# Optimization experiments

Measured on AMD Instinct MI355X. Metric: run time of the kernel, lower is better.

## Reference

```python
import jax, jax.numpy as jnp
import numpy as np

K_NEIGHBORS = 20


def _glorot(key, shape):
    fan_in = shape[0]
    return jax.random.normal(key, shape, dtype=jnp.float32) / jnp.sqrt(jnp.float32(fan_in))


def setup_inputs() -> dict:
    key = jax.random.key(0)
    ks = jax.random.split(key, 20)
    B, N, D = 16, 1024, 3
    out_channels = 40
    pos = jax.random.normal(ks[0], (B, N, D), dtype=jnp.float32)
    inp = {
        "pos": pos,
        # conv1 MLP: [6 -> 64 -> 64 -> 64]
        "W1a": _glorot(ks[1], (6, 64)),   "b1a": jnp.zeros((64,), jnp.float32),
        "W1b": _glorot(ks[2], (64, 64)),  "b1b": jnp.zeros((64,), jnp.float32),
        "W1c": _glorot(ks[3], (64, 64)),  "b1c": jnp.zeros((64,), jnp.float32),
        # conv2 MLP: [128 -> 128]
        "W2": _glorot(ks[4], (128, 128)), "b2": jnp.zeros((128,), jnp.float32),
        # lin1: 64+128 -> 1024
        "Wl": _glorot(ks[5], (192, 1024)), "bl": jnp.zeros((1024,), jnp.float32),
        # head MLP: [1024 -> 512 -> 256 -> out]
        "Wm1": _glorot(ks[6], (1024, 512)), "bm1": jnp.zeros((512,), jnp.float32),
        "Wm2": _glorot(ks[7], (512, 256)),  "bm2": jnp.zeros((256,), jnp.float32),
        "Wm3": _glorot(ks[8], (256, out_channels)), "bm3": jnp.zeros((out_channels,), jnp.float32),
    }
    return inp


def _knn_idx(x, k):
    # x: [B, N, D] -> idx: [B, N, k] of nearest neighbors (self excluded)
    sq = jnp.sum(x * x, axis=-1)                      # [B, N]
    d = sq[:, :, None] + sq[:, None, :] - 2.0 * jnp.einsum("bnd,bmd->bnm", x, x)
    n = x.shape[1]
    d = d + jnp.eye(n, dtype=d.dtype)[None] * jnp.float32(1e10)  # exclude self
    _, idx = jax.lax.top_k(-d, k)                     # smallest distances
    return idx


def _edge_conv(x, k, mlp_fn):
    # DynamicEdgeConv: kNN graph on current features, message = mlp([x_i, x_j - x_i]), max-aggr.
    idx = _knn_idx(x, k)                              # [B, N, k]
    nb = jax.vmap(lambda xb, ib: xb[ib])(x, idx)      # [B, N, k, C] gather
    xi = jnp.broadcast_to(x[:, :, None, :], nb.shape)
    e = jnp.concatenate([xi, nb - xi], axis=-1)       # [B, N, k, 2C]
    return jnp.max(mlp_fn(e), axis=2)                 # max over neighbors -> [B, N, C']


def reference(pos, W1a, b1a, W1b, b1b, W1c, b1c, W2, b2, Wl, bl,
              Wm1, bm1, Wm2, bm2, Wm3, bm3):
    relu = jax.nn.relu
    # conv1: MLP([6,64,64,64]) -- ReLU after hidden layers, plain last (eval: BN identity, dropout off)
    mlp1 = lambda e: relu(relu(e @ W1a + b1a) @ W1b + b1b) @ W1c + b1c
    x1 = _edge_conv(pos, K_NEIGHBORS, mlp1)           # [B, N, 64]
    # conv2: MLP([128,128]) -- single plain linear
    x2 = _edge_conv(x1, K_NEIGHBORS, lambda e: e @ W2 + b2)  # [B, N, 128]
    out = jnp.concatenate([x1, x2], axis=-1) @ Wl + bl       # [B, N, 1024]
    g = jnp.max(out, axis=1)                                  # global max pool -> [B, 1024]
    h = relu(g @ Wm1 + bm1)
    h = relu(h @ Wm2 + bm2)
    logits = h @ Wm3 + bm3                                    # [B, 40]
    return jax.nn.log_softmax(logits, axis=1)
```

## Files before the change

kernel.cpp:

```cpp
#include <hip/hip_runtime.h>

constexpr int NB  = 16;
constexpr int NP  = 1024;
constexpr int NPT = NB * NP;
constexpr int KNB = 20;

typedef unsigned short ushortT;
typedef __bf16 bf16x8 __attribute__((ext_vector_type(8)));
typedef _Float16 f16x8 __attribute__((ext_vector_type(8)));
typedef float f32x4 __attribute__((ext_vector_type(4)));

__device__ inline unsigned f2bf_pair(float f0, float f1) {
    unsigned u0 = __float_as_uint(f0); u0 = (u0 + 0x7FFFu + ((u0 >> 16) & 1u)) >> 16;
    unsigned u1 = __float_as_uint(f1); u1 = (u1 + 0x7FFFu + ((u1 >> 16) & 1u)) >> 16;
    return u0 | (u1 << 16);
}

__device__ inline unsigned monokey(float f) {
    unsigned u = __float_as_uint(f);
    return u ^ ((unsigned)((int)u >> 31) | 0x80000000u);
}

__device__ inline unsigned dppmin16(unsigned v) {
    unsigned t;
    t = (unsigned)__builtin_amdgcn_update_dpp((int)v, (int)v, 0xB1, 0xF, 0xF, false);
    v = v < t ? v : t;
    t = (unsigned)__builtin_amdgcn_update_dpp((int)v, (int)v, 0x4E, 0xF, 0xF, false);
    v = v < t ? v : t;
    t = (unsigned)__builtin_amdgcn_update_dpp((int)v, (int)v, 0x141, 0xF, 0xF, false);
    v = v < t ? v : t;
    t = (unsigned)__builtin_amdgcn_update_dpp((int)v, (int)v, 0x140, 0xF, 0xF, false);
    v = v < t ? v : t;
    return v;
}

__device__ inline void sort16_u64(unsigned long long key[16]) {
#pragma unroll
    for (int k = 2; k <= 16; k <<= 1) {
#pragma unroll
        for (int j = k >> 1; j > 0; j >>= 1) {
#pragma unroll
            for (int a = 0; a < 16; ++a) {
                int b = a ^ j;
                if (b > a) {
                    unsigned long long x = key[a], y = key[b];
                    bool lt = x < y;
                    unsigned long long mn = lt ? x : y, mx = lt ? y : x;
                    if ((a & k) == 0) { key[a] = mn; key[b] = mx; }
                    else              { key[a] = mx; key[b] = mn; }
                }
            }
        }
    }
}

__device__ inline void wave_top20_lds(unsigned long long key[16], int lane,
                                      unsigned long long* __restrict__ col,
                                      int* __restrict__ outp, int jadd)
{
    sort16_u64(key);
#pragma unroll
    for (int s = 0; s < 16; ++s) col[s] = key[s];
    unsigned ptr = 0;
    for (int t = 0; t < KNB; ++t) {
        unsigned long long h = col[ptr];
        unsigned hv = (unsigned)(h >> 32);
        unsigned hj = (unsigned)h;
        unsigned r = dppmin16(hv);
        unsigned g0 = (unsigned)__builtin_amdgcn_readlane((int)r, 0);
        unsigned g1 = (unsigned)__builtin_amdgcn_readlane((int)r, 16);
        unsigned g2 = (unsigned)__builtin_amdgcn_readlane((int)r, 32);
        unsigned g3 = (unsigned)__builtin_amdgcn_readlane((int)r, 48);
        unsigned g = min(min(g0, g1), min(g2, g3));
        unsigned long long ball = __ballot(hv == g);
        int wl = __ffsll(ball) - 1;
        int wj = __builtin_amdgcn_readlane((int)hj, wl);
        if (lane == 0) outp[t] = jadd + wj;
        ptr += (lane == wl) ? 1u : 0u;
    }
}

__device__ inline void tourney20(unsigned long long key[16], int lane,
                                 unsigned long long* __restrict__ heap,
                                 int* __restrict__ outp, int jadd)
{
    sort16_u64(key);
#pragma unroll
    for (int s = 0; s < 16; ++s)
        heap[lane * 16 + ((s + lane) & 15)] = key[s];
    unsigned ptr = 0;
    for (int t = 0; t < KNB; ++t) {
        unsigned pcl = ptr < 15u ? ptr : 15u;
        unsigned long long h = heap[lane * 16 + (((int)pcl + lane) & 15)];
        if (ptr >= 16u) h = ~0ULL;
        unsigned hv = (unsigned)(h >> 32);
        unsigned hj = (unsigned)h;
        unsigned r = dppmin16(hv);
        unsigned g0 = (unsigned)__builtin_amdgcn_readlane((int)r, 0);
        unsigned g1 = (unsigned)__builtin_amdgcn_readlane((int)r, 16);
        unsigned g2 = (unsigned)__builtin_amdgcn_readlane((int)r, 32);
        unsigned g3 = (unsigned)__builtin_amdgcn_readlane((int)r, 48);
        unsigned g = min(min(g0, g1), min(g2, g3));
        unsigned long long ball = __ballot(hv == g);
        int wl = __ffsll(ball) - 1;
        int wj = __builtin_amdgcn_readlane((int)hj, wl);
        if (lane == 0) outp[t] = jadd + wj;
        ptr += (lane == wl) ? 1u : 0u;
    }
}

__global__ void fail_kernel(float* out, int n) {
    int i = blockIdx.x * 256 + threadIdx.x;
    if (i < n) out[i] = -777.0f;
}

__global__ __launch_bounds__(256) void prep_w_kernel(
    const float* __restrict__ W2,
    const float* __restrict__ Wm1, const float* __restrict__ Wm2, const float* __restrict__ Wm3,
    const float* __restrict__ Wl, const float* __restrict__ W1b, const float* __restrict__ W1c,
    float* __restrict__ Wcat, float* __restrict__ Wm1T, float* __restrict__ Wm2T, float* __restrict__ Wm3T,
    ushortT* __restrict__ Wlb, _Float16* __restrict__ Wc1f)
{
    int id = blockIdx.x * 256 + threadIdx.x;
    if (id < 64 * 256) {
        int c = id >> 8, n = id & 255;
        float wb = W2[(64 + c) * 128 + (n & 127)];
        Wcat[id] = (n < 128) ? wb : (W2[c * 128 + (n - 128)] - wb);
        return;
    }
    id -= 64 * 256;
    if (id < 512 * 1024) { int j = id >> 10, c = id & 1023; Wm1T[id] = Wm1[c * 512 + j]; return; }
    id -= 512 * 1024;
    if (id < 256 * 512)  { int j = id >> 9,  c = id & 511;  Wm2T[id] = Wm2[c * 256 + j]; return; }
    id -= 256 * 512;
    if (id < 40 * 256)   { int j = id >> 8,  c = id & 255;  Wm3T[id] = Wm3[c * 40 + j];  return; }
    id -= 40 * 256;
    if (id < 8 * 6 * 8 * 64 * 8) {
        int j = id & 7;
        int t = id >> 3;
        int lane = t & 63; t >>= 6;
        int f = t & 7; t >>= 3;
        int s = t % 6, nt = t / 6;
        int k = s * 32 + (lane >> 4) * 8 + j;
        int n = nt * 128 + f * 16 + (lane & 15);
        unsigned u = __float_as_uint(Wl[(size_t)k * 1024 + n]);
        u = (u + 0x7FFFu + ((u >> 16) & 1u)) >> 16;
        Wlb[id] = (ushortT)u;
        return;
    }
    id -= 8 * 6 * 8 * 64 * 8;
    if (id < 16384) {
        int mat = id >> 13;
        int rem = id & 8191;
        int part = rem >> 12;
        int t = rem & 4095;
        int frag = t >> 9;
        int r = t & 511;
        int lane = r >> 3, j = r & 7;
        int kf = frag >> 2, nf = frag & 3;
        int k = kf * 32 + (lane >> 4) * 8 + j;
        int n = nf * 16 + (lane & 15);
        float w = (mat ? W1c : W1b)[k * 64 + n];
        _Float16 hi = (_Float16)w;
        Wc1f[id] = part ? (_Float16)(w - (float)hi) : hi;
        return;
    }
}

__global__ __launch_bounds__(256) void prep_uv1_kernel(
    const float* __restrict__ pos, const float* __restrict__ W1a, const float* __restrict__ b1a,
    float* __restrict__ u1, float* __restrict__ v1)
{
    int id = blockIdx.x * 256 + threadIdx.x;
    int i = id >> 6, c = id & 63;
    float x = pos[3 * i], y = pos[3 * i + 1], z = pos[3 * i + 2];
    float wu0 = W1a[3 * 64 + c], wu1 = W1a[4 * 64 + c], wu2 = W1a[5 * 64 + c];
    float wv0 = W1a[0 * 64 + c] - wu0, wv1 = W1a[1 * 64 + c] - wu1, wv2 = W1a[2 * 64 + c] - wu2;
    u1[id] = x * wu0 + y * wu1 + z * wu2;
    v1[id] = b1a[c] + x * wv0 + y * wv1 + z * wv2;
}

__global__ __launch_bounds__(256) void knn3_kernel(const float* __restrict__ pos, int* __restrict__ idx)
{
    __shared__ unsigned long long heap[4][64][17];
    const int tid = threadIdx.x;
    const int w = tid >> 6, lane = tid & 63;
    const int b = blockIdx.x >> 8;
    const int i = ((blockIdx.x & 255) << 2) + w;
    const float* pb = pos + (size_t)b * NP * 3;

    float cbuf[48];
    {
        const float4* src = (const float4*)(pb + lane * 48);
#pragma unroll
        for (int q = 0; q < 12; ++q) *(float4*)&cbuf[q * 4] = src[q];
    }
    const float xi = pb[3 * i], yi = pb[3 * i + 1], zi = pb[3 * i + 2];
    const float sqi = xi * xi + yi * yi + zi * zi;
    unsigned long long key[16];
#pragma unroll
    for (int s = 0; s < 16; ++s) {
        float x = cbuf[3 * s], y = cbuf[3 * s + 1], z = cbuf[3 * s + 2];
        float d = sqi + (x * x + y * y + z * z) - 2.0f * (xi * x + yi * y + zi * z);
        int j = (lane << 4) + s;
        if (j == i) d += 1e10f;
        key[s] = ((unsigned long long)monokey(d) << 32) | (unsigned)j;
    }
    heap[w][lane][16] = ~0ULL;
    wave_top20_lds(key, lane, &heap[w][lane][0], idx + (size_t)(b * NP + i) * KNB, b * NP);
}

__global__ __launch_bounds__(64, 1) void conv1_mfma_kernel(
    const int* __restrict__ idx, const float* __restrict__ u1, const float* __restrict__ v1,
    const _Float16* __restrict__ Wf, const float* __restrict__ b1b, const float* __restrict__ b1c,
    float* __restrict__ x1)
{
    __shared__ int idx_s[16 * 20];
    __shared__ __align__(16) float tr[16 * 68];
    __shared__ __align__(16) float xout[16 * 68];
    const int lane = threadIdx.x;
    const int row = lane & 15, ks = lane >> 4;
    const int pbase = blockIdx.x * 16;

    for (int t = lane; t < 320; t += 64) idx_s[t] = idx[(size_t)pbase * 20 + t];

    const f16x8* Wp = (const f16x8*)Wf;
    f16x8 wbh[2][4], wbl[2][4], wch[2][4], wcl[2][4];
#pragma unroll
    for (int kf = 0; kf < 2; ++kf)
#pragma unroll
        for (int nf = 0; nf < 4; ++nf) {
            int f = kf * 4 + nf;
            wbh[kf][nf] = Wp[(0 * 8 + f) * 64 + lane];
            wbl[kf][nf] = Wp[(1 * 8 + f) * 64 + lane];
            wch[kf][nf] = Wp[(2 * 8 + f) * 64 + lane];
            wcl[kf][nf] = Wp[(3 * 8 + f) * 64 + lane];
        }
    float bb[4], bc[4];
#pragma unroll
    for (int nf = 0; nf < 4; ++nf) { bb[nf] = b1b[nf * 16 + row]; bc[nf] = b1c[nf * 16 + row]; }

    const int P = pbase + row;
    float4 v1f[4];
    {
        const float4* v4a = (const float4*)(v1 + (size_t)P * 64 + ks * 8);
        v1f[0] = v4a[0]; v1f[1] = v4a[1];
        const float4* v4b = (const float4*)(v1 + (size_t)P * 64 + 32 + ks * 8);
        v1f[2] = v4b[0]; v1f[3] = v4b[1];
    }
    f32x4 xmax[4];
#pragma unroll
    for (int nf = 0; nf < 4; ++nf) xmax[nf] = (f32x4)(-3.0e38f);

    int jn = idx_s[row * 20];
    float4 un[4];
    {
        const float4* up = (const float4*)(u1 + (size_t)jn * 64 + ks * 8);
        un[0] = up[0]; un[1] = up[1];
        const float4* up2 = (const float4*)(u1 + (size_t)jn * 64 + 32 + ks * 8);
        un[2] = up2[0]; un[3] = up2[1];
    }
    for (int e = 0; e < 20; ++e) {
        float4 uc[4] = {un[0], un[1], un[2], un[3]};
        if (e < 19) {
            jn = idx_s[row * 20 + e + 1];
            const float4* up = (const float4*)(u1 + (size_t)jn * 64 + ks * 8);
            un[0] = up[0]; un[1] = up[1];
            const float4* up2 = (const float4*)(u1 + (size_t)jn * 64 + 32 + ks * 8);
            un[2] = up2[0]; un[3] = up2[1];
        }
        f32x4 c2[4];
#pragma unroll
        for (int nf = 0; nf < 4; ++nf) c2[nf] = (f32x4)(bb[nf]);
#pragma unroll
        for (int kf = 0; kf < 2; ++kf) {
            const float* uu = (const float*)&uc[kf * 2];
            const float* vv = (const float*)&v1f[kf * 2];
            f16x8 ah, al;
#pragma unroll
            for (int q = 0; q < 8; ++q) {
                float h = fmaxf(uu[q] + vv[q], 0.f);
                _Float16 hi = (_Float16)h;
                ah[q] = hi;
                al[q] = (_Float16)(h - (float)hi);
            }
#pragma unroll
            for (int nf = 0; nf < 4; ++nf) {
                c2[nf] = __builtin_amdgcn_mfma_f32_16x16x32_f16(ah, wbh[kf][nf], c2[nf], 0, 0, 0);
                c2[nf] = __builtin_amdgcn_mfma_f32_16x16x32_f16(ah, wbl[kf][nf], c2[nf], 0, 0, 0);
                c2[nf] = __builtin_amdgcn_mfma_f32_16x16x32_f16(al, wbh[kf][nf], c2[nf], 0, 0, 0);
            }
        }
#pragma unroll
        for (int nf = 0; nf < 4; ++nf)
#pragma unroll
            for (int r = 0; r < 4; ++r)
                tr[(ks * 4 + r) * 68 + nf * 16 + row] = fmaxf(c2[nf][r], 0.f);
        __builtin_amdgcn_sched_barrier(0);
        f32x4 c3[4];
#pragma unroll
        for (int nf = 0; nf < 4; ++nf) c3[nf] = (f32x4)0.0f;
#pragma unroll
        for (int kf = 0; kf < 2; ++kf) {
            float hbuf[8];
            *(float4*)&hbuf[0] = *(const float4*)&tr[row * 68 + kf * 32 + ks * 8];
            *(float4*)&hbuf[4] = *(const float4*)&tr[row * 68 + kf * 32 + ks * 8 + 4];
            f16x8 ah, al;
#pragma unroll
            for (int q = 0; q < 8; ++q) {
                _Float16 hi = (_Float16)hbuf[q];
                ah[q] = hi;
                al[q] = (_Float16)(hbuf[q] - (float)hi);
            }
#pragma unroll
            for (int nf = 0; nf < 4; ++nf) {
                c3[nf] = __builtin_amdgcn_mfma_f32_16x16x32_f16(ah, wch[kf][nf], c3[nf], 0, 0, 0);
                c3[nf] = __builtin_amdgcn_mfma_f32_16x16x32_f16(ah, wcl[kf][nf], c3[nf], 0, 0, 0);
                c3[nf] = __builtin_amdgcn_mfma_f32_16x16x32_f16(al, wch[kf][nf], c3[nf], 0, 0, 0);
            }
        }
        __builtin_amdgcn_sched_barrier(0);
#pragma unroll
        for (int nf = 0; nf < 4; ++nf) {
            xmax[nf][0] = fmaxf(xmax[nf][0], c3[nf][0]);
            xmax[nf][1] = fmaxf(xmax[nf][1], c3[nf][1]);
            xmax[nf][2] = fmaxf(xmax[nf][2], c3[nf][2]);
            xmax[nf][3] = fmaxf(xmax[nf][3], c3[nf][3]);
        }
    }
#pragma unroll
    for (int nf = 0; nf < 4; ++nf)
#pragma unroll
        for (int r = 0; r < 4; ++r)
            xout[(ks * 4 + r) * 68 + nf * 16 + row] = xmax[nf][r] + bc[nf];
    __builtin_amdgcn_sched_barrier(0);
    {
        const int r2 = lane >> 2, c0 = (lane & 3) * 16;
#pragma unroll
        for (int q = 0; q < 4; ++q) {
            float4 v = *(const float4*)&xout[r2 * 68 + c0 + q * 4];
            *(float4*)(x1 + (size_t)(pbase + r2) * 64 + c0 + q * 4) = v;
        }
    }
}

__global__ __launch_bounds__(256) void sqnorm_kernel(
    const float* __restrict__ x1, float* __restrict__ sq,
    ushortT* __restrict__ Afrag, _Float16* __restrict__ Xf)
{
    int i = blockIdx.x * 256 + threadIdx.x;
    const float4* r = (const float4*)(x1 + (size_t)i * 64);
    float c[64];
    float s = 0.f;
#pragma unroll
    for (int q = 0; q < 16; ++q) {
        float4 a = r[q];
        c[4 * q] = a.x; c[4 * q + 1] = a.y; c[4 * q + 2] = a.z; c[4 * q + 3] = a.w;
        s += a.x * a.x + a.y * a.y + a.z * a.z + a.w * a.w;
    }
    sq[i] = s;
    const size_t t = i >> 4;
#pragma unroll
    for (int cb = 0; cb < 8; ++cb) {
        uint4 pk;
        pk.x = f2bf_pair(c[8 * cb + 0], c[8 * cb + 1]);
        pk.y = f2bf_pair(c[8 * cb + 2], c[8 * cb + 3]);
        pk.z = f2bf_pair(c[8 * cb + 4], c[8 * cb + 5]);
        pk.w = f2bf_pair(c[8 * cb + 6], c[8 * cb + 7]);
        size_t af = (t * 6 + (cb >> 2)) * 512 + (size_t)((cb & 3) * 16 + (i & 15)) * 8;
        *(uint4*)(Afrag + af) = pk;
        int kf = cb >> 2;
        int lanef = ((cb & 3) << 4) + (i & 15);
        __align__(16) _Float16 hbuf[8];
        __align__(16) _Float16 lbuf[8];
#pragma unroll
        for (int q2 = 0; q2 < 8; ++q2) {
            float v = c[cb * 8 + q2];
            _Float16 hi = (_Float16)v;
            hbuf[q2] = hi;
            lbuf[q2] = (_Float16)(v - (float)hi);
        }
        *(uint4*)(Xf + ((t * 2 + kf) * 2 + 0) * 512 + (size_t)lanef * 8) = *(uint4*)hbuf;
        *(uint4*)(Xf + ((t * 2 + kf) * 2 + 1) * 512 + (size_t)lanef * 8) = *(uint4*)lbuf;
    }
}

__global__ __launch_bounds__(512, 4) void dist2sel_kernel(
    const _Float16* __restrict__ Xf, const float* __restrict__ sq, int* __restrict__ idx)
{
    __shared__ unsigned kls[16 * 1032];
    const int tid = threadIdx.x;
    const int w = tid >> 6, lane = tid & 63;
    const int b = blockIdx.x >> 6;
    const int rowtile = blockIdx.x & 63;
    const int c15 = lane & 15;
    const int rbase = (lane >> 4) * 4;

    const f16x8* Xv = (const f16x8*)Xf;
    const int tA = b * 64 + rowtile;
    f16x8 ah[2], al[2];
#pragma unroll
    for (int kf = 0; kf < 2; ++kf) {
        ah[kf] = Xv[((size_t)(tA * 2 + kf) * 2 + 0) * 64 + lane];
        al[kf] = Xv[((size_t)(tA * 2 + kf) * 2 + 1) * 64 + lane];
    }
    const float* sqb = sq + (size_t)b * NP;
    float sqi[4];
#pragma unroll
    for (int rr = 0; rr < 4; ++rr)
        sqi[rr] = sqb[rowtile * 16 + rbase + rr];

    for (int q = 0; q < 8; ++q) {
        const int ct = w * 8 + q;
        const int tB = b * 64 + ct;
        f16x8 bh0 = Xv[((size_t)(tB * 2 + 0) * 2 + 0) * 64 + lane];
        f16x8 bl0 = Xv[((size_t)(tB * 2 + 0) * 2 + 1) * 64 + lane];
        f16x8 bh1 = Xv[((size_t)(tB * 2 + 1) * 2 + 0) * 64 + lane];
        f16x8 bl1 = Xv[((size_t)(tB * 2 + 1) * 2 + 1) * 64 + lane];
        const int col = ct * 16 + c15;
        const float sqj = sqb[col];
        f32x4 acc = (f32x4)0.0f;
        acc = __builtin_amdgcn_mfma_f32_16x16x32_f16(ah[0], bh0, acc, 0, 0, 0);
        acc = __builtin_amdgcn_mfma_f32_16x16x32_f16(ah[0], bl0, acc, 0, 0, 0);
        acc = __builtin_amdgcn_mfma_f32_16x16x32_f16(al[0], bh0, acc, 0, 0, 0);
        acc = __builtin_amdgcn_mfma_f32_16x16x32_f16(ah[1], bh1, acc, 0, 0, 0);
        acc = __builtin_amdgcn_mfma_f32_16x16x32_f16(ah[1], bl1, acc, 0, 0, 0);
        acc = __builtin_amdgcn_mfma_f32_16x16x32_f16(al[1], bh1, acc, 0, 0, 0);
        const int pc = col ^ (((col >> 6) & 7) << 1);
#pragma unroll
        for (int rr = 0; rr < 4; ++rr) {
            float d = sqi[rr] + sqj - 2.0f * acc[rr];
            if (rowtile * 16 + rbase + rr == col) d += 1e10f;
            kls[(rbase + rr) * 1032 + pc] = monokey(d);
        }
    }
    __syncthreads();

    const int r0 = 2 * w, r1 = 2 * w + 1;
    unsigned kv0[16], kv1[16];
#pragma unroll
    for (int s = 0; s < 16; ++s) {
        int col = (lane << 4) + s;
        int pc = col ^ (((col >> 6) & 7) << 1);
        kv0[s] = kls[r0 * 1032 + pc];
        kv1[s] = kls[r1 * 1032 + pc];
    }
    unsigned long long* heap = (unsigned long long*)&kls[(size_t)w * 2 * 1032];
    const int gb = b * NP;
    {
        unsigned long long key[16];
#pragma unroll
        for (int s = 0; s < 16; ++s)
            key[s] = ((unsigned long long)kv0[s] << 32) | (unsigned)((lane << 4) + s);
        tourney20(key, lane, heap, idx + (size_t)(gb + rowtile * 16 + r0) * KNB, gb);
    }
    {
        unsigned long long key[16];
#pragma unroll
        for (int s = 0; s < 16; ++s)
            key[s] = ((unsigned long long)kv1[s] << 32) | (unsigned)((lane << 4) + s);
        tourney20(key, lane, heap, idx + (size_t)(gb + rowtile * 16 + r1) * KNB, gb);
    }
}

__global__ __launch_bounds__(256) void u2v2_kernel(
    const float* __restrict__ x1, const float* __restrict__ Wcat, const float* __restrict__ b2,
    float* __restrict__ u2, float* __restrict__ v2)
{
    __shared__ float aT[32][132];
    __shared__ float bW[32][132];
    const int tid = threadIdx.x;
    const int mt = blockIdx.x >> 1, nt = blockIdx.x & 1;
    const int m0 = mt << 7, n0 = nt << 7;
    const int ti = tid >> 4, tj = tid & 15;
    float acc[8][8];
#pragma unroll
    for (int a = 0; a < 8; ++a)
#pragma unroll
        for (int q = 0; q < 8; ++q) acc[a][q] = 0.f;
    for (int ct = 0; ct < 2; ++ct) {
        __syncthreads();
#pragma unroll
        for (int rep = 0; rep < 4; ++rep) {
            int f = tid + (rep << 8);
            { int r = f >> 3, q = f & 7;
              float4 v = *(const float4*)(x1 + (size_t)(m0 + r) * 64 + ct * 32 + q * 4);
              aT[4 * q + 0][r] = v.x; aT[4 * q + 1][r] = v.y; aT[4 * q + 2][r] = v.z; aT[4 * q + 3][r] = v.w; }
            { int cc = f >> 5, q = f & 31;
              *(float4*)&bW[cc][4 * q] = *(const float4*)(Wcat + (size_t)(ct * 32 + cc) * 256 + n0 + q * 4); }
        }
        __syncthreads();
#pragma unroll 4
        for (int c = 0; c < 32; ++c) {
            float af[8], bf[8];
            *(float4*)&af[0] = *(const float4*)&aT[c][ti * 8];
            *(float4*)&af[4] = *(const float4*)&aT[c][ti * 8 + 4];
            *(float4*)&bf[0] = *(const float4*)&bW[c][tj * 8];
            *(float4*)&bf[4] = *(const float4*)&bW[c][tj * 8 + 4];
#pragma unroll
            for (int a = 0; a < 8; ++a)
#pragma unroll
                for (int q = 0; q < 8; ++q) acc[a][q] = fmaf(af[a], bf[q], acc[a][q]);
        }
    }
#pragma unroll
    for (int a = 0; a < 8; ++a) {
        int m = m0 + ti * 8 + a;
        if (n0 < 128) {
            float outv[8];
#pragma unroll
            for (int q = 0; q < 8; ++q) outv[q] = acc[a][q];
            *(float4*)(u2 + (size_t)m * 128 + n0 + tj * 8)     = *(float4*)&outv[0];
            *(float4*)(u2 + (size_t)m * 128 + n0 + tj * 8 + 4) = *(float4*)&outv[4];
        } else {
            float outv[8];
#pragma unroll
            for (int q = 0; q < 8; ++q) outv[q] = acc[a][q] + b2[n0 - 128 + tj * 8 + q];
            *(float4*)(v2 + (size_t)m * 128 + (n0 - 128) + tj * 8)     = *(float4*)&outv[0];
            *(float4*)(v2 + (size_t)m * 128 + (n0 - 128) + tj * 8 + 4) = *(float4*)&outv[4];
        }
    }
}

__global__ __launch_bounds__(256) void gatherfrag_kernel(
    const int* __restrict__ idx, const float* __restrict__ u2,
    const float* __restrict__ v2, ushortT* __restrict__ Afrag)
{
    const int tid = threadIdx.x;
    const int i = blockIdx.x * 16 + (tid >> 4);
    const int cb = tid & 15;
    const int* ib = idx + (size_t)i * KNB;
    float m[8];
#pragma unroll
    for (int d = 0; d < 8; ++d) m[d] = -3e38f;
    for (int e = 0; e < KNB; ++e) {
        int j = ib[e];
        const float4* p = (const float4*)(u2 + (size_t)j * 128 + cb * 8);
        float4 a = p[0], b = p[1];
        m[0] = fmaxf(m[0], a.x); m[1] = fmaxf(m[1], a.y); m[2] = fmaxf(m[2], a.z); m[3] = fmaxf(m[3], a.w);
        m[4] = fmaxf(m[4], b.x); m[5] = fmaxf(m[5], b.y); m[6] = fmaxf(m[6], b.z); m[7] = fmaxf(m[7], b.w);
    }
    const float4* vp = (const float4*)(v2 + (size_t)i * 128 + cb * 8);
    float4 va = vp[0], vb = vp[1];
    m[0] += va.x; m[1] += va.y; m[2] += va.z; m[3] += va.w;
    m[4] += vb.x; m[5] += vb.y; m[6] += vb.z; m[7] += vb.w;
    uint4 pk;
    pk.x = f2bf_pair(m[0], m[1]);
    pk.y = f2bf_pair(m[2], m[3]);
    pk.z = f2bf_pair(m[4], m[5]);
    pk.w = f2bf_pair(m[6], m[7]);
    size_t af = ((size_t)(i >> 4) * 6 + 2 + (cb >> 2)) * 512 + (size_t)((cb & 3) * 16 + (i & 15)) * 8;
    *(uint4*)(Afrag + af) = pk;
}

__global__ __launch_bounds__(256) void lin1max_mfma_kernel(
    const ushortT* __restrict__ Afrag, const ushortT* __restrict__ Wlb, float* __restrict__ gp)
{
    __shared__ float red[4][128];
    const int tid = threadIdx.x;
    const int w = tid >> 6, lane = tid & 63;
    const int nt = blockIdx.x & 7;
    const int rt = (blockIdx.x >> 3) & 7;
    const int b  = blockIdx.x >> 6;
    const int rt16 = ((b << 3) + rt) * 8 + (w << 1);
    const bf16x8* Ap = (const bf16x8*)Afrag;
    const bf16x8* Bp = (const bf16x8*)Wlb;
    f32x4 acc[2][8];
#pragma unroll
    for (int mm = 0; mm < 2; ++mm)
#pragma unroll
        for (int f = 0; f < 8; ++f) acc[mm][f] = (f32x4)0.0f;
#pragma unroll
    for (int s = 0; s < 6; ++s) {
        bf16x8 a0 = Ap[((rt16    ) * 6 + s) * 64 + lane];
        bf16x8 a1 = Ap[((rt16 + 1) * 6 + s) * 64 + lane];
#pragma unroll
        for (int f = 0; f < 8; ++f) {
            bf16x8 bb = Bp[(((nt * 6 + s) << 3) + f) * 64 + lane];
            acc[0][f] = __builtin_amdgcn_mfma_f32_16x16x32_bf16(a0, bb, acc[0][f], 0, 0, 0);
            acc[1][f] = __builtin_amdgcn_mfma_f32_16x16x32_bf16(a1, bb, acc[1][f], 0, 0, 0);
        }
    }
#pragma unroll
    for (int f = 0; f < 8; ++f) {
        float m = acc[0][f][0];
        m = fmaxf(m, acc[0][f][1]); m = fmaxf(m, acc[0][f][2]); m = fmaxf(m, acc[0][f][3]);
        m = fmaxf(m, acc[1][f][0]); m = fmaxf(m, acc[1][f][1]);
        m = fmaxf(m, acc[1][f][2]); m = fmaxf(m, acc[1][f][3]);
        m = fmaxf(m, __shfl_xor(m, 16, 64));
        m = fmaxf(m, __shfl_xor(m, 32, 64));
        if (lane < 16) red[w][f * 16 + lane] = m;
    }
    __syncthreads();
    if (tid < 128) {
        float m = fmaxf(fmaxf(red[0][tid], red[1][tid]), fmaxf(red[2][tid], red[3][tid]));
        gp[((size_t)rt * NB + b) * 1024 + nt * 128 + tid] = m;
    }
}

__global__ __launch_bounds__(256) void gmax_kernel(
    const float* __restrict__ gp, const float* __restrict__ bl, float* __restrict__ gs)
{
    int id = blockIdx.x * 256 + threadIdx.x;
    int b = id >> 10, c = id & 1023;
    float m = gp[(size_t)b * 1024 + c];
#pragma unroll
    for (int part = 1; part < 8; ++part)
        m = fmaxf(m, gp[((size_t)part * NB + b) * 1024 + c]);
    gs[(size_t)b * 1024 + c] = m + bl[c];
}

__global__ __launch_bounds__(256) void head1_kernel(
    const float* __restrict__ gs, const float* __restrict__ Wm1T, const float* __restrict__ bm1,
    float* __restrict__ h1)
{
    __shared__ float red[16][17];
    const int j = blockIdx.x;
    const int t = threadIdx.x;
    const int b = t >> 4, seg = t & 15;
    const float4* wr = (const float4*)(Wm1T + (size_t)j * 1024 + seg * 64);
    const float4* gr = (const float4*)(gs + (size_t)b * 1024 + seg * 64);
    float acc = 0.f;
#pragma unroll
    for (int q = 0; q < 16; ++q) {
        float4 w = wr[q], g = gr[q];
        acc = fmaf(w.x, g.x, acc); acc = fmaf(w.y, g.y, acc);
        acc = fmaf(w.z, g.z, acc); acc = fmaf(w.w, g.w, acc);
    }
    red[b][seg] = acc;
    __syncthreads();
    if (t < 16) {
        float s = 0.f;
#pragma unroll
        for (int k = 0; k < 16; ++k) s += red[t][k];
        h1[(size_t)t * 512 + j] = fmaxf(s + bm1[j], 0.f);
    }
}

__global__ __launch_bounds__(256) void head2_kernel(
    const float* __restrict__ h1, const float* __restrict__ Wm2T, const float* __restrict__ bm2,
    float* __restrict__ h2)
{
    __shared__ float red[16][17];
    const int j = blockIdx.x;
    const int t = threadIdx.x;
    const int b = t >> 4, seg = t & 15;
    const float4* wr = (const float4*)(Wm2T + (size_t)j * 512 + seg * 32);
    const float4* hr = (const float4*)(h1 + (size_t)b * 512 + seg * 32);
    float acc = 0.f;
#pragma unroll
    for (int q = 0; q < 8; ++q) {
        float4 w = wr[q], g = hr[q];
        acc = fmaf(w.x, g.x, acc); acc = fmaf(w.y, g.y, acc);
        acc = fmaf(w.z, g.z, acc); acc = fmaf(w.w, g.w, acc);
    }
    red[b][seg] = acc;
    __syncthreads();
    if (t < 16) {
        float s = 0.f;
#pragma unroll
        for (int k = 0; k < 16; ++k) s += red[t][k];
        h2[(size_t)t * 256 + j] = fmaxf(s + bm2[j], 0.f);
    }
}

__global__ __launch_bounds__(256) void head3_kernel(
    const float* __restrict__ h2, const float* __restrict__ Wm3T, const float* __restrict__ bm3,
    float* __restrict__ out)
{
    __shared__ float lg[64];
    const int tid = threadIdx.x;
    const int b = blockIdx.x;
    if (tid < 40) {
        float acc = bm3[tid];
        const float4* wr = (const float4*)(Wm3T + (size_t)tid * 256);
        const float4* hr = (const float4*)(h2 + (size_t)b * 256);
#pragma unroll
        for (int c4 = 0; c4 < 64; ++c4) {
            float4 w = wr[c4];
            float4 g4 = hr[c4];
            acc = fmaf(w.x, g4.x, acc); acc = fmaf(w.y, g4.y, acc);
            acc = fmaf(w.z, g4.z, acc); acc = fmaf(w.w, g4.w, acc);
        }
        lg[tid] = acc;
    }
    __syncthreads();
    if (tid < 64) {
        float v = (tid < 40) ? lg[tid] : -3e38f;
        float m = v;
        for (int off = 32; off; off >>= 1) m = fmaxf(m, __shfl_xor(m, off, 64));
        float ex = (tid < 40) ? expf(v - m) : 0.f;
        float s = ex;
        for (int off = 32; off; off >>= 1) s += __shfl_xor(s, off, 64);
        if (tid < 40) out[b * 40 + tid] = v - m - logf(s);
    }
}

extern "C" void kernel_launch(void* const* d_in, const int* in_sizes, int n_in,
                              void* d_out, int out_size, void* d_ws, size_t ws_size,
                              hipStream_t stream)
{
    const float* pos = (const float*)d_in[0];
    const float* W1a = (const float*)d_in[1];
    const float* b1a = (const float*)d_in[2];
    const float* W1b = (const float*)d_in[3];
    const float* b1b = (const float*)d_in[4];
    const float* W1c = (const float*)d_in[5];
    const float* b1c = (const float*)d_in[6];
    const float* W2  = (const float*)d_in[7];
    const float* b2  = (const float*)d_in[8];
    const float* Wl  = (const float*)d_in[9];
    const float* bl  = (const float*)d_in[10];
    const float* Wm1 = (const float*)d_in[11];
    const float* bm1 = (const float*)d_in[12];
    const float* Wm2 = (const float*)d_in[13];
    const float* bm2 = (const float*)d_in[14];
    const float* Wm3 = (const float*)d_in[15];
    const float* bm3 = (const float*)d_in[16];
    float* out = (float*)d_out;

    char* ws = (char*)d_ws;
    const size_t MB = 1024 * 1024;
    size_t off = 0;
    auto alloc = [&](size_t bytes) { size_t o = off; off += (bytes + 255) & ~(size_t)255; return o; };
    size_t u2_off  = alloc(8 * MB);
    size_t v2_off  = alloc(8 * MB);
    size_t x1_off  = alloc(4 * MB);
    size_t idx_off = alloc((size_t)NPT * KNB * 4);
    size_t sq_off  = alloc((size_t)NPT * 4);
    size_t gp_off  = alloc((size_t)8 * NB * 1024 * 4);
    size_t gs_off  = alloc((size_t)NB * 1024 * 4);
    size_t h1_off  = alloc((size_t)NB * 512 * 4);
    size_t h2_off  = alloc((size_t)NB * 256 * 4);
    size_t wc_off  = alloc(64 * 256 * 4);
    size_t w1t_off = alloc(512 * 1024 * 4);
    size_t w2t_off = alloc(256 * 512 * 4);
    size_t w3t_off = alloc(40 * 256 * 4);
    size_t af_off  = alloc((size_t)(NPT / 16) * 6 * 512 * 2);
    size_t wlb_off = alloc((size_t)8 * 6 * 8 * 512 * 2);
    size_t wcf_off = alloc((size_t)16384 * 2);
    size_t xf_off  = alloc((size_t)(NPT / 16) * 2 * 2 * 512 * 2);
    if (ws_size < off) { fail_kernel<<<3, 256, 0, stream>>>(out, out_size); return; }

    float* u1    = (float*)(ws + u2_off);
    float* v1    = (float*)(ws + v2_off);
    float* u2    = (float*)(ws + u2_off);
    float* v2    = (float*)(ws + v2_off);
    float* x1    = (float*)(ws + x1_off);
    int*   idx   = (int*)(ws + idx_off);
    float* sq    = (float*)(ws + sq_off);
    float* gp    = (float*)(ws + gp_off);
    float* gs    = (float*)(ws + gs_off);
    float* h1    = (float*)(ws + h1_off);
    float* h2    = (float*)(ws + h2_off);
    float* Wcat  = (float*)(ws + wc_off);
    float* Wm1T  = (float*)(ws + w1t_off);
    float* Wm2T  = (float*)(ws + w2t_off);
    float* Wm3T  = (float*)(ws + w3t_off);
    ushortT* Afrag = (ushortT*)(ws + af_off);
    ushortT* Wlb   = (ushortT*)(ws + wlb_off);
    _Float16* Wc1f = (_Float16*)(ws + wcf_off);
    _Float16* Xf   = (_Float16*)(ws + xf_off);

    prep_w_kernel<<<3496, 256, 0, stream>>>(W2, Wm1, Wm2, Wm3, Wl, W1b, W1c,
                                            Wcat, Wm1T, Wm2T, Wm3T, Wlb, Wc1f);
    prep_uv1_kernel<<<4096, 256, 0, stream>>>(pos, W1a, b1a, u1, v1);
    knn3_kernel<<<4096, 256, 0, stream>>>(pos, idx);
    conv1_mfma_kernel<<<1024, 64, 0, stream>>>(idx, u1, v1, Wc1f, b1b, b1c, x1);
    sqnorm_kernel<<<64, 256, 0, stream>>>(x1, sq, Afrag, Xf);
    dist2sel_kernel<<<1024, 512, 0, stream>>>(Xf, sq, idx);
    u2v2_kernel<<<256, 256, 0, stream>>>(x1, Wcat, b2, u2, v2);
    gatherfrag_kernel<<<1024, 256, 0, stream>>>(idx, u2, v2, Afrag);
    lin1max_mfma_kernel<<<1024, 256, 0, stream>>>(Afrag, Wlb, gp);
    gmax_kernel<<<64, 256, 0, stream>>>(gp, bl, gs);
    head1_kernel<<<512, 256, 0, stream>>>(gs, Wm1T, bm1, h1);
    head2_kernel<<<256, 256, 0, stream>>>(h1, Wm2T, bm2, h2);
    head3_kernel<<<16, 256, 0, stream>>>(h2, Wm3T, bm3, out);
}
```

Before: 192.9 us.

## Merge prep and kNN kernels into one launch; use 32-bit keys in dist2sel tourney

```diff
diff --git a/kernel.cpp b/kernel.cpp
--- a/kernel.cpp
+++ b/kernel.cpp
@@ -80,48 +80,60 @@
     }
 }
 
-__device__ inline void tourney20(unsigned long long key[16], int lane,
-                                 unsigned long long* __restrict__ heap,
-                                 int* __restrict__ outp, int jadd)
-{
-    sort16_u64(key);
-#pragma unroll
-    for (int s = 0; s < 16; ++s)
-        heap[lane * 16 + ((s + lane) & 15)] = key[s];
-    unsigned ptr = 0;
-    for (int t = 0; t < KNB; ++t) {
-        unsigned pcl = ptr < 15u ? ptr : 15u;
-        unsigned long long h = heap[lane * 16 + (((int)pcl + lane) & 15)];
-        if (ptr >= 16u) h = ~0ULL;
-        unsigned hv = (unsigned)(h >> 32);
-        unsigned hj = (unsigned)h;
-        unsigned r = dppmin16(hv);
-        unsigned g0 = (unsigned)__builtin_amdgcn_readlane((int)r, 0);
-        unsigned g1 = (unsigned)__builtin_amdgcn_readlane((int)r, 16);
-        unsigned g2 = (unsigned)__builtin_amdgcn_readlane((int)r, 32);
-        unsigned g3 = (unsigned)__builtin_amdgcn_readlane((int)r, 48);
-        unsigned g = min(min(g0, g1), min(g2, g3));
-        unsigned long long ball = __ballot(hv == g);
-        int wl = __ffsll(ball) - 1;
-        int wj = __builtin_amdgcn_readlane((int)hj, wl);
-        if (lane == 0) outp[t] = jadd + wj;
-        ptr += (lane == wl) ? 1u : 0u;
-    }
-}
-
 __global__ void fail_kernel(float* out, int n) {
     int i = blockIdx.x * 256 + threadIdx.x;
     if (i < n) out[i] = -777.0f;
 }
 
-__global__ __launch_bounds__(256) void prep_w_kernel(
+__global__ __launch_bounds__(256) void phase1_kernel(
+    const float* __restrict__ pos, const float* __restrict__ W1a, const float* __restrict__ b1a,
     const float* __restrict__ W2,
     const float* __restrict__ Wm1, const float* __restrict__ Wm2, const float* __restrict__ Wm3,
     const float* __restrict__ Wl, const float* __restrict__ W1b, const float* __restrict__ W1c,
+    int* __restrict__ idx, float* __restrict__ u1, float* __restrict__ v1,
     float* __restrict__ Wcat, float* __restrict__ Wm1T, float* __restrict__ Wm2T, float* __restrict__ Wm3T,
     ushortT* __restrict__ Wlb, _Float16* __restrict__ Wc1f)
 {
-    int id = blockIdx.x * 256 + threadIdx.x;
+    __shared__ unsigned long long heap[4][64][17];
+    const int bid = blockIdx.x;
+    const int tid = threadIdx.x;
+    if (bid < 4096) {
+        const int w = tid >> 6, lane = tid & 63;
+        const int b = bid >> 8;
+        const int i = ((bid & 255) << 2) + w;
+        const float* pb = pos + (size_t)b * NP * 3;
+        float cbuf[48];
+        {
+            const float4* src = (const float4*)(pb + lane * 48);
+#pragma unroll
+            for (int q = 0; q < 12; ++q) *(float4*)&cbuf[q * 4] = src[q];
+        }
+        const float xi = pb[3 * i], yi = pb[3 * i + 1], zi = pb[3 * i + 2];
+        const float sqi = xi * xi + yi * yi + zi * zi;
+        unsigned long long key[16];
+#pragma unroll
+        for (int s = 0; s < 16; ++s) {
+            float x = cbuf[3 * s], y = cbuf[3 * s + 1], z = cbuf[3 * s + 2];
+            float d = sqi + (x * x + y * y + z * z) - 2.0f * (xi * x + yi * y + zi * z);
+            int j = (lane << 4) + s;
+            if (j == i) d += 1e10f;
+            key[s] = ((unsigned long long)monokey(d) << 32) | (unsigned)j;
+        }
+        heap[w][lane][16] = ~0ULL;
+        wave_top20_lds(key, lane, &heap[w][lane][0], idx + (size_t)(b * NP + i) * KNB, b * NP);
+        return;
+    }
+    if (bid < 8192) {
+        int id = (bid - 4096) * 256 + tid;
+        int i = id >> 6, c = id & 63;
+        float x = pos[3 * i], y = pos[3 * i + 1], z = pos[3 * i + 2];
+        float wu0 = W1a[3 * 64 + c], wu1 = W1a[4 * 64 + c], wu2 = W1a[5 * 64 + c];
+        float wv0 = W1a[0 * 64 + c] - wu0, wv1 = W1a[1 * 64 + c] - wu1, wv2 = W1a[2 * 64 + c] - wu2;
+        u1[id] = x * wu0 + y * wu1 + z * wu2;
+        v1[id] = b1a[c] + x * wv0 + y * wv1 + z * wv2;
+        return;
+    }
+    int id = (bid - 8192) * 256 + tid;
     if (id < 64 * 256) {
         int c = id >> 8, n = id & 255;
         float wb = W2[(64 + c) * 128 + (n & 127)];
@@ -167,49 +179,6 @@
     }
 }
 
-__global__ __launch_bounds__(256) void prep_uv1_kernel(
-    const float* __restrict__ pos, const float* __restrict__ W1a, const float* __restrict__ b1a,
-    float* __restrict__ u1, float* __restrict__ v1)
-{
-    int id = blockIdx.x * 256 + threadIdx.x;
-    int i = id >> 6, c = id & 63;
-    float x = pos[3 * i], y = pos[3 * i + 1], z = pos[3 * i + 2];
-    float wu0 = W1a[3 * 64 + c], wu1 = W1a[4 * 64 + c], wu2 = W1a[5 * 64 + c];
-    float wv0 = W1a[0 * 64 + c] - wu0, wv1 = W1a[1 * 64 + c] - wu1, wv2 = W1a[2 * 64 + c] - wu2;
-    u1[id] = x * wu0 + y * wu1 + z * wu2;
-    v1[id] = b1a[c] + x * wv0 + y * wv1 + z * wv2;
-}
-
-__global__ __launch_bounds__(256) void knn3_kernel(const float* __restrict__ pos, int* __restrict__ idx)
-{
-    __shared__ unsigned long long heap[4][64][17];
-    const int tid = threadIdx.x;
-    const int w = tid >> 6, lane = tid & 63;
-    const int b = blockIdx.x >> 8;
-    const int i = ((blockIdx.x & 255) << 2) + w;
-    const float* pb = pos + (size_t)b * NP * 3;
-
-    float cbuf[48];
-    {
-        const float4* src = (const float4*)(pb + lane * 48);
-#pragma unroll
-        for (int q = 0; q < 12; ++q) *(float4*)&cbuf[q * 4] = src[q];
-    }
-    const float xi = pb[3 * i], yi = pb[3 * i + 1], zi = pb[3 * i + 2];
-    const float sqi = xi * xi + yi * yi + zi * zi;
-    unsigned long long key[16];
-#pragma unroll
-    for (int s = 0; s < 16; ++s) {
-        float x = cbuf[3 * s], y = cbuf[3 * s + 1], z = cbuf[3 * s + 2];
-        float d = sqi + (x * x + y * y + z * z) - 2.0f * (xi * x + yi * y + zi * z);
-        int j = (lane << 4) + s;
-        if (j == i) d += 1e10f;
-        key[s] = ((unsigned long long)monokey(d) << 32) | (unsigned)j;
-    }
-    heap[w][lane][16] = ~0ULL;
-    wave_top20_lds(key, lane, &heap[w][lane][0], idx + (size_t)(b * NP + i) * KNB, b * NP);
-}
-
 __global__ __launch_bounds__(64, 1) void conv1_mfma_kernel(
     const int* __restrict__ idx, const float* __restrict__ u1, const float* __restrict__ v1,
     const _Float16* __restrict__ Wf, const float* __restrict__ b1b, const float* __restrict__ b1c,
@@ -436,30 +405,48 @@
     }
     __syncthreads();
 
-    const int r0 = 2 * w, r1 = 2 * w + 1;
-    unsigned kv0[16], kv1[16];
-#pragma unroll
-    for (int s = 0; s < 16; ++s) {
-        int col = (lane << 4) + s;
-        int pc = col ^ (((col >> 6) & 7) << 1);
-        kv0[s] = kls[r0 * 1032 + pc];
-        kv1[s] = kls[r1 * 1032 + pc];
-    }
-    unsigned long long* heap = (unsigned long long*)&kls[(size_t)w * 2 * 1032];
     const int gb = b * NP;
-    {
+    for (int rr2 = 0; rr2 < 2; ++rr2) {
+        const int r = 2 * w + rr2;
+        unsigned kv[16];
+#pragma unroll
+        for (int s = 0; s < 16; ++s) {
+            int col = (lane << 4) + s;
+            int pc = col ^ (((col >> 6) & 7) << 1);
+            kv[s] = kls[r * 1032 + pc];
+        }
         unsigned long long key[16];
 #pragma unroll
         for (int s = 0; s < 16; ++s)
-            key[s] = ((unsigned long long)kv0[s] << 32) | (unsigned)((lane << 4) + s);
-        tourney20(key, lane, heap, idx + (size_t)(gb + rowtile * 16 + r0) * KNB, gb);
-    }
-    {
-        unsigned long long key[16];
-#pragma unroll
-        for (int s = 0; s < 16; ++s)
-            key[s] = ((unsigned long long)kv1[s] << 32) | (unsigned)((lane << 4) + s);
-        tourney20(key, lane, heap, idx + (size_t)(gb + rowtile * 16 + r1) * KNB, gb);
+            key[s] = ((unsigned long long)kv[s] << 32) | (unsigned)((lane << 4) + s);
+        sort16_u64(key);
+        unsigned* hrow = &kls[r * 1032];
+        unsigned long long perm = 0;
+#pragma unroll
+        for (int p = 0; p < 16; ++p) {
+            hrow[lane * 16 + ((p + lane) & 15)] = (unsigned)(key[p] >> 32);
+            perm |= (unsigned long long)((unsigned)key[p] & 15u) << (4 * p);
+        }
+        unsigned ptr = 0;
+        int* outp = idx + (size_t)(gb + rowtile * 16 + r) * KNB;
+        for (int t = 0; t < KNB; ++t) {
+            unsigned pcl = ptr < 15u ? ptr : 15u;
+            unsigned hv = hrow[lane * 16 + (((int)pcl + lane) & 15)];
+            if (ptr >= 16u) hv = 0xFFFFFFFFu;
+            unsigned rm = dppmin16(hv);
+            unsigned g0 = (unsigned)__builtin_amdgcn_readlane((int)rm, 0);
+            unsigned g1 = (unsigned)__builtin_amdgcn_readlane((int)rm, 16);
+            unsigned g2 = (unsigned)__builtin_amdgcn_readlane((int)rm, 32);
+            unsigned g3 = (unsigned)__builtin_amdgcn_readlane((int)rm, 48);
+            unsigned g = min(min(g0, g1), min(g2, g3));
+            unsigned long long ball = __ballot(hv == g);
+            int wl = __ffsll(ball) - 1;
+            int sor = (int)((perm >> (4 * (int)pcl)) & 15ull);
+            int j = (lane << 4) + sor;
+            int wj = __builtin_amdgcn_readlane(j, wl);
+            if (lane == 0) outp[t] = gb + wj;
+            ptr += (lane == wl) ? 1u : 0u;
+        }
     }
 }
 
@@ -762,10 +749,8 @@
     _Float16* Wc1f = (_Float16*)(ws + wcf_off);
     _Float16* Xf   = (_Float16*)(ws + xf_off);
 
-    prep_w_kernel<<<3496, 256, 0, stream>>>(W2, Wm1, Wm2, Wm3, Wl, W1b, W1c,
-                                            Wcat, Wm1T, Wm2T, Wm3T, Wlb, Wc1f);
-    prep_uv1_kernel<<<4096, 256, 0, stream>>>(pos, W1a, b1a, u1, v1);
-    knn3_kernel<<<4096, 256, 0, stream>>>(pos, idx);
+    phase1_kernel<<<11688, 256, 0, stream>>>(pos, W1a, b1a, W2, Wm1, Wm2, Wm3, Wl, W1b, W1c,
+                                             idx, u1, v1, Wcat, Wm1T, Wm2T, Wm3T, Wlb, Wc1f);
     conv1_mfma_kernel<<<1024, 64, 0, stream>>>(idx, u1, v1, Wc1f, b1b, b1c, x1);
     sqnorm_kernel<<<64, 256, 0, stream>>>(x1, sq, Afrag, Xf);
     dist2sel_kernel<<<1024, 512, 0, stream>>>(Xf, sq, idx);
```

Result: faster. 187.4 us (-2.8%).
